# Kernel optimization log

Measured on AMD Instinct MI355X. Metric: run time of the kernel, lower is better.

The kernel has to match this reference:

```python
import jax, jax.numpy as jnp
import numpy as np

B, C, H, W = 16, 128, 128, 128
K = 3          # kernel_size
RED = 8        # CA reduction


def setup_inputs() -> dict:
    key = jax.random.key(0)
    ks = jax.random.split(key, 8)
    s = 0.05
    return {
        "x0": jax.random.normal(ks[0], (B, C, H, W), jnp.float32),
        "deg": jax.random.normal(ks[1], (B, C), jnp.float32),
        # kernel-generating MLP (torch Linear weights: (out, in), no bias)
        "w1": jax.random.normal(ks[2], (C, C), jnp.float32) * s,
        "w2": jax.random.normal(ks[3], (C * K * K, C), jnp.float32) * s,
        # 1x1 conv (with bias)
        "conv_w": jax.random.normal(ks[4], (C, C, 1, 1), jnp.float32) * s,
        "conv_b": jax.random.normal(ks[5], (C,), jnp.float32) * s,
        # CA layer 1x1 convs (no bias)
        "ca_w1": jax.random.normal(ks[6], (C // RED, C, 1, 1), jnp.float32) * s,
        "ca_w2": jax.random.normal(ks[7], (C, C // RED, 1, 1), jnp.float32) * s,
    }


def _lrelu(v):
    return jax.nn.leaky_relu(v, 0.1)


def reference(x0, deg, w1, w2, conv_w, conv_b, ca_w1, ca_w2):
    b, c, h, w = x0.shape
    # dynamic per-sample depthwise kernels: (b, C*K*K) -> (b*C, 1, K, K)
    kern = (_lrelu(deg @ w1.T) @ w2.T).reshape(b * c, 1, K, K)
    pad = (K - 1) // 2
    # grouped conv with groups = b*c (per-sample depthwise)
    out = jax.lax.conv_general_dilated(
        x0.reshape(1, b * c, h, w), kern,
        window_strides=(1, 1), padding=[(pad, pad), (pad, pad)],
        feature_group_count=b * c,
        dimension_numbers=("NCHW", "OIHW", "NCHW"))
    out = _lrelu(out).reshape(b, c, h, w)
    # 1x1 conv with bias
    out = jnp.einsum("bchw,oc->bohw", out, conv_w[:, :, 0, 0]) + conv_b[None, :, None, None]
    # CA attention from degradation rep (all 1x1 convs on a 1x1 map == matmuls)
    att = jax.nn.sigmoid(
        jnp.einsum("br,or->bo", _lrelu(jnp.einsum("bc,rc->br", deg, ca_w1[:, :, 0, 0])),
                   ca_w2[:, :, 0, 0]))
    return out + x0 * att[:, :, None, None]
```

## Files before the change

### kernel.cpp

```cpp
#include <hip/hip_runtime.h>
#include <hip/hip_bf16.h>
#include <stdint.h>

static constexpr int BB = 16, CC_ = 128, HH = 128, WW = 128;

typedef float  f32x4 __attribute__((ext_vector_type(4)));
typedef short  s16x8 __attribute__((ext_vector_type(8)));
typedef uint32_t u32x4 __attribute__((ext_vector_type(4)));

__device__ __forceinline__ uint16_t f2bf(float f) {
    union { float f; uint32_t u; } a; a.f = f;
    uint32_t r = a.u + 0x7FFFu + ((a.u >> 16) & 1u);
    return (uint16_t)(r >> 16);
}

__device__ __forceinline__ float lrelu(float v) { return fmaxf(v, 0.1f * v); }

__global__ __launch_bounds__(128) void prep_kernel(
    const float* __restrict__ deg, const float* __restrict__ w1,
    const float* __restrict__ w2, const float* __restrict__ conv_w,
    const float* __restrict__ ca_w1, const float* __restrict__ ca_w2,
    float* __restrict__ kern_ws, float* __restrict__ att_ws,
    uint16_t* __restrict__ Wp)
{
    const int t = threadIdx.x;
    if (blockIdx.x < 16) {
        const int b = blockIdx.x;
        __shared__ float sdeg[128];
        __shared__ float shid[128];
        __shared__ float sh2[16];
        sdeg[t] = deg[b * 128 + t];
        __syncthreads();
        {
            float acc = 0.f;
            const float* w1r = w1 + t * 128;
            for (int c = 0; c < 128; ++c) acc += sdeg[c] * w1r[c];
            shid[t] = lrelu(acc);
        }
        if (t < 16) {
            float a2 = 0.f;
            const float* cw = ca_w1 + t * 128;
            for (int c = 0; c < 128; ++c) a2 += sdeg[c] * cw[c];
            sh2[t] = lrelu(a2);
        }
        __syncthreads();
        {
            float aa = 0.f;
            const float* c2 = ca_w2 + t * 16;
            #pragma unroll
            for (int r = 0; r < 16; ++r) aa += sh2[r] * c2[r];
            att_ws[b * 128 + t] = 1.f / (1.f + expf(-aa));
        }
        for (int j = 0; j < 9; ++j) {
            float kv = 0.f;
            const float* w2r = w2 + (t * 9 + j) * 128;
            for (int r = 0; r < 128; ++r) kv += shid[r] * w2r[r];
            kern_ws[(b * 128 + t) * 12 + j] = kv;
        }
        kern_ws[(b * 128 + t) * 12 + 9]  = 0.f;
        kern_ws[(b * 128 + t) * 12 + 10] = 0.f;
        kern_ws[(b * 128 + t) * 12 + 11] = 0.f;
    } else {
        for (int idx = t; idx < 16384; idx += 128) {
            int j    = idx & 7;
            int lane = (idx >> 3) & 63;
            int kk   = (idx >> 9) & 3;
            int mt   = idx >> 11;
            int o = mt * 16 + (lane & 15);
            int c = kk * 32 + ((lane >> 4) & 3) * 8 + j;
            Wp[idx] = f2bf(conv_w[o * 128 + c]);
        }
    }
}

__global__ __launch_bounds__(256, 2) void main_kernel(
    const float* __restrict__ x0, const float* __restrict__ kern_ws,
    const float* __restrict__ att_ws, const uint16_t* __restrict__ Wp,
    const float* __restrict__ conv_b, float* __restrict__ out)
{
    __shared__ uint16_t y_s[128 * 128];

    const int bid = blockIdx.x;
    const int lg  = (bid & 7) * 256 + (bid >> 3);
    const int b = lg >> 7;
    const int h = lg & 127;

    const int t    = threadIdx.x;
    const int lane = t & 63;
    const int q    = t >> 6;
    const int c0   = (t >> 4) * 8;
    const int w0   = (t & 15) * 8;

    float kf[8][9];
    #pragma unroll
    for (int cc = 0; cc < 8; ++cc) {
        const float* kp = kern_ws + (b * 128 + c0 + cc) * 12;
        f32x4 ka = *(const f32x4*)kp;
        f32x4 kb = *(const f32x4*)(kp + 4);
        float k8 = kp[8];
        kf[cc][0] = ka.x; kf[cc][1] = ka.y; kf[cc][2] = ka.z; kf[cc][3] = ka.w;
        kf[cc][4] = kb.x; kf[cc][5] = kb.y; kf[cc][6] = kb.z; kf[cc][7] = kb.w;
        kf[cc][8] = k8;
    }

    uint32_t ypk[8][4];
    #pragma unroll
    for (int cc = 0; cc < 8; ++cc) {
        const int c = c0 + cc;
        const float* xpl = x0 + (b * 128 + c) * (128 * 128);
        float a8[8];
        #pragma unroll
        for (int i = 0; i < 8; ++i) a8[i] = 0.f;
        #pragma unroll
        for (int dr = 0; dr < 3; ++dr) {
            const int r = h - 1 + dr;
            f32x4 f0, f1;
            if ((unsigned)r < 128u) {
                const float* rp = xpl + r * 128 + w0;
                f0 = *(const f32x4*)rp;
                f1 = *(const f32x4*)(rp + 4);
            } else {
                f0.x = f0.y = f0.z = f0.w = 0.f;
                f1.x = f1.y = f1.z = f1.w = 0.f;
            }
            float lft = __shfl(f1.w, (lane - 1) & 63);
            float rgt = __shfl(f0.x, (lane + 1) & 63);
            if ((t & 15) == 0)  lft = 0.f;
            if ((t & 15) == 15) rgt = 0.f;
            const float k0 = kf[cc][dr * 3 + 0];
            const float k1 = kf[cc][dr * 3 + 1];
            const float k2 = kf[cc][dr * 3 + 2];
            a8[0] += k0 * lft  + k1 * f0.x + k2 * f0.y;
            a8[1] += k0 * f0.x + k1 * f0.y + k2 * f0.z;
            a8[2] += k0 * f0.y + k1 * f0.z + k2 * f0.w;
            a8[3] += k0 * f0.z + k1 * f0.w + k2 * f1.x;
            a8[4] += k0 * f0.w + k1 * f1.x + k2 * f1.y;
            a8[5] += k0 * f1.x + k1 * f1.y + k2 * f1.z;
            a8[6] += k0 * f1.y + k1 * f1.z + k2 * f1.w;
            a8[7] += k0 * f1.z + k1 * f1.w + k2 * rgt;
        }
        #pragma unroll
        for (int wi = 0; wi < 8; ++wi) {
            uint32_t u = f2bf(lrelu(a8[wi]));
            if ((cc & 1) == 0) ypk[wi][cc >> 1] = u;
            else               ypk[wi][cc >> 1] |= (u << 16);
        }
    }
    #pragma unroll
    for (int wi = 0; wi < 8; ++wi) {
        const int w = w0 + wi;
        int off = w * 256 + c0 * 2;
        off ^= (((w & 7) ^ ((w >> 3) & 7)) << 4);
        u32x4 v; v.x = ypk[wi][0]; v.y = ypk[wi][1]; v.z = ypk[wi][2]; v.w = ypk[wi][3];
        *(u32x4*)((char*)y_s + off) = v;
    }

    const int ah = q >> 1;
    const int nh = q & 1;
    s16x8 Af[4][4];
    #pragma unroll
    for (int mt = 0; mt < 4; ++mt)
        #pragma unroll
        for (int kk = 0; kk < 4; ++kk)
            Af[mt][kk] = *(const s16x8*)(Wp + (((ah * 4 + mt) * 4 + kk) * 64 + lane) * 8);

    float cbv[4][4], atv[4][4];
    #pragma unroll
    for (int mt = 0; mt < 4; ++mt)
        #pragma unroll
        for (int r = 0; r < 4; ++r) {
            const int o = (ah * 4 + mt) * 16 + (lane >> 4) * 4 + r;
            cbv[mt][r] = conv_b[o];
            atv[mt][r] = att_ws[b * 128 + o];
        }

    __syncthreads();

    f32x4 acc[4][4];
    #pragma unroll
    for (int mt = 0; mt < 4; ++mt)
        #pragma unroll
        for (int nt = 0; nt < 4; ++nt) {
            acc[mt][nt].x = cbv[mt][0];
            acc[mt][nt].y = cbv[mt][1];
            acc[mt][nt].z = cbv[mt][2];
            acc[mt][nt].w = cbv[mt][3];
        }

    #pragma unroll
    for (int nt = 0; nt < 4; ++nt) {
        const int w = (nh * 4 + nt) * 16 + (lane & 15);
        const int swz = (((w & 7) ^ ((w >> 3) & 7)) << 4);
        #pragma unroll
        for (int kk = 0; kk < 4; ++kk) {
            const int off = (w * 256 + kk * 64 + (lane >> 4) * 16) ^ swz;
            s16x8 Bf = *(const s16x8*)((const char*)y_s + off);
            #pragma unroll
            for (int mt = 0; mt < 4; ++mt)
                acc[mt][nt] = __builtin_amdgcn_mfma_f32_16x16x32_bf16(
                    Af[mt][kk], Bf, acc[mt][nt], 0, 0, 0);
        }
    }

    #pragma unroll
    for (int mt = 0; mt < 4; ++mt)
        #pragma unroll
        for (int nt = 0; nt < 4; ++nt) {
            const int w = (nh * 4 + nt) * 16 + (lane & 15);
            #pragma unroll
            for (int r = 0; r < 4; ++r) {
                const int o = (ah * 4 + mt) * 16 + (lane >> 4) * 4 + r;
                const int idx = ((b * 128 + o) * 128 + h) * 128 + w;
                out[idx] = acc[mt][nt][r] + x0[idx] * atv[mt][r];
            }
        }
}

extern "C" void kernel_launch(void* const* d_in, const int* in_sizes, int n_in,
                              void* d_out, int out_size, void* d_ws, size_t ws_size,
                              hipStream_t stream) {
    const float* x0     = (const float*)d_in[0];
    const float* deg    = (const float*)d_in[1];
    const float* w1     = (const float*)d_in[2];
    const float* w2     = (const float*)d_in[3];
    const float* conv_w = (const float*)d_in[4];
    const float* conv_b = (const float*)d_in[5];
    const float* ca_w1  = (const float*)d_in[6];
    const float* ca_w2  = (const float*)d_in[7];
    float* out = (float*)d_out;

    float* kern_ws = (float*)d_ws;
    float* att_ws  = kern_ws + 16 * 128 * 12;
    uint16_t* Wp   = (uint16_t*)(att_ws + 16 * 128);

    prep_kernel<<<17, 128, 0, stream>>>(deg, w1, w2, conv_w, ca_w1, ca_w2,
                                        kern_ws, att_ws, Wp);
    main_kernel<<<2048, 256, 0, stream>>>(x0, kern_ws, att_ws, Wp, conv_b, out);
}
```

Baseline: 432.7 us.

## Split prep kernel, stage epilogue through LDS for coalesced stores, raise occupancy

The serial per-sample w2 projection is moved out of the 17-block prep kernel into a second, wider kernel that uses vectorized row dot products. In the main kernel the MFMA operand roles are swapped so the output tile lands in LDS as [o][w]. It is then written back in two halves with 16-byte coalesced loads of x0 and stores to out, replacing scattered scalar accesses. Launch bounds rise to 4 blocks per SM, which trades more barriers and register pressure for occupancy and an extra kernel launch.

```diff
diff --git a/kernel.cpp b/kernel.cpp
--- a/kernel.cpp
+++ b/kernel.cpp
@@ -1,8 +1,6 @@
 #include <hip/hip_runtime.h>
 #include <hip/hip_bf16.h>
 #include <stdint.h>
-
-static constexpr int BB = 16, CC_ = 128, HH = 128, WW = 128;
 
 typedef float  f32x4 __attribute__((ext_vector_type(4)));
 typedef short  s16x8 __attribute__((ext_vector_type(8)));
@@ -13,21 +11,19 @@
     uint32_t r = a.u + 0x7FFFu + ((a.u >> 16) & 1u);
     return (uint16_t)(r >> 16);
 }
-
 __device__ __forceinline__ float lrelu(float v) { return fmaxf(v, 0.1f * v); }
 
-__global__ __launch_bounds__(128) void prep_kernel(
+__global__ __launch_bounds__(128) void prep1_kernel(
     const float* __restrict__ deg, const float* __restrict__ w1,
-    const float* __restrict__ w2, const float* __restrict__ conv_w,
-    const float* __restrict__ ca_w1, const float* __restrict__ ca_w2,
-    float* __restrict__ kern_ws, float* __restrict__ att_ws,
+    const float* __restrict__ conv_w, const float* __restrict__ ca_w1,
+    const float* __restrict__ ca_w2,
+    float* __restrict__ hid_ws, float* __restrict__ att_ws,
     uint16_t* __restrict__ Wp)
 {
     const int t = threadIdx.x;
     if (blockIdx.x < 16) {
         const int b = blockIdx.x;
         __shared__ float sdeg[128];
-        __shared__ float shid[128];
         __shared__ float sh2[16];
         sdeg[t] = deg[b * 128 + t];
         __syncthreads();
@@ -35,7 +31,7 @@
             float acc = 0.f;
             const float* w1r = w1 + t * 128;
             for (int c = 0; c < 128; ++c) acc += sdeg[c] * w1r[c];
-            shid[t] = lrelu(acc);
+            hid_ws[b * 128 + t] = lrelu(acc);
         }
         if (t < 16) {
             float a2 = 0.f;
@@ -51,34 +47,54 @@
             for (int r = 0; r < 16; ++r) aa += sh2[r] * c2[r];
             att_ws[b * 128 + t] = 1.f / (1.f + expf(-aa));
         }
-        for (int j = 0; j < 9; ++j) {
-            float kv = 0.f;
-            const float* w2r = w2 + (t * 9 + j) * 128;
-            for (int r = 0; r < 128; ++r) kv += shid[r] * w2r[r];
-            kern_ws[(b * 128 + t) * 12 + j] = kv;
-        }
-        kern_ws[(b * 128 + t) * 12 + 9]  = 0.f;
-        kern_ws[(b * 128 + t) * 12 + 10] = 0.f;
-        kern_ws[(b * 128 + t) * 12 + 11] = 0.f;
     } else {
         for (int idx = t; idx < 16384; idx += 128) {
             int j    = idx & 7;
             int lane = (idx >> 3) & 63;
             int kk   = (idx >> 9) & 3;
-            int mt   = idx >> 11;
-            int o = mt * 16 + (lane & 15);
+            int ot   = idx >> 11;
+            int o = ot * 16 + (lane & 15);
             int c = kk * 32 + ((lane >> 4) & 3) * 8 + j;
             Wp[idx] = f2bf(conv_w[o * 128 + c]);
         }
     }
 }
 
-__global__ __launch_bounds__(256, 2) void main_kernel(
+__global__ __launch_bounds__(256) void prep2_kernel(
+    const float* __restrict__ hid_ws, const float* __restrict__ w2,
+    float* __restrict__ kern_ws)
+{
+    const int b  = blockIdx.x;
+    const int cj = blockIdx.y * 256 + threadIdx.x;
+    __shared__ f32x4 shid[32];
+    if (threadIdx.x < 32)
+        shid[threadIdx.x] = *(const f32x4*)(hid_ws + b * 128 + threadIdx.x * 4);
+    __syncthreads();
+    if (cj < 1152) {
+        const int c = cj / 9, j = cj - c * 9;
+        const f32x4* row = (const f32x4*)(w2 + cj * 128);
+        float acc = 0.f;
+        #pragma unroll 8
+        for (int r = 0; r < 32; ++r) {
+            f32x4 a = shid[r], v = row[r];
+            acc += a.x * v.x + a.y * v.y + a.z * v.z + a.w * v.w;
+        }
+        kern_ws[(b * 128 + c) * 12 + j] = acc;
+    } else {
+        const int z = cj - 1152;
+        const int c = z / 3, j = 9 + (z - (z / 3) * 3);
+        kern_ws[(b * 128 + c) * 12 + j] = 0.f;
+    }
+}
+
+__global__ __launch_bounds__(256, 4) void main_kernel(
     const float* __restrict__ x0, const float* __restrict__ kern_ws,
     const float* __restrict__ att_ws, const uint16_t* __restrict__ Wp,
     const float* __restrict__ conv_b, float* __restrict__ out)
 {
-    __shared__ uint16_t y_s[128 * 128];
+    __shared__ char smem[64 * 132 * 4];
+    uint16_t* y_s   = (uint16_t*)smem;
+    float*    ystage = (float*)smem;
 
     const int bid = blockIdx.x;
     const int lg  = (bid & 7) * 256 + (bid >> 3);
@@ -97,10 +113,9 @@
         const float* kp = kern_ws + (b * 128 + c0 + cc) * 12;
         f32x4 ka = *(const f32x4*)kp;
         f32x4 kb = *(const f32x4*)(kp + 4);
-        float k8 = kp[8];
         kf[cc][0] = ka.x; kf[cc][1] = ka.y; kf[cc][2] = ka.z; kf[cc][3] = ka.w;
         kf[cc][4] = kb.x; kf[cc][5] = kb.y; kf[cc][6] = kb.z; kf[cc][7] = kb.w;
-        kf[cc][8] = k8;
+        kf[cc][8] = kp[8];
     }
 
     uint32_t ypk[8][4];
@@ -155,65 +170,78 @@
         *(u32x4*)((char*)y_s + off) = v;
     }
 
-    const int ah = q >> 1;
-    const int nh = q & 1;
-    s16x8 Af[4][4];
+    const int mh = q >> 1;
+    const int oh = q & 1;
+    s16x8 Bf[4][4];
+    #pragma unroll
+    for (int nt = 0; nt < 4; ++nt)
+        #pragma unroll
+        for (int kk = 0; kk < 4; ++kk)
+            Bf[nt][kk] = *(const s16x8*)(Wp + (((oh * 4 + nt) * 4 + kk) * 64 + lane) * 8);
+    float cb[4];
+    #pragma unroll
+    for (int nt = 0; nt < 4; ++nt)
+        cb[nt] = conv_b[(oh * 4 + nt) * 16 + (lane & 15)];
+
+    __syncthreads();
+
+    f32x4 acc[4][4];
     #pragma unroll
     for (int mt = 0; mt < 4; ++mt)
         #pragma unroll
-        for (int kk = 0; kk < 4; ++kk)
-            Af[mt][kk] = *(const s16x8*)(Wp + (((ah * 4 + mt) * 4 + kk) * 64 + lane) * 8);
-
-    float cbv[4][4], atv[4][4];
-    #pragma unroll
-    for (int mt = 0; mt < 4; ++mt)
-        #pragma unroll
-        for (int r = 0; r < 4; ++r) {
-            const int o = (ah * 4 + mt) * 16 + (lane >> 4) * 4 + r;
-            cbv[mt][r] = conv_b[o];
-            atv[mt][r] = att_ws[b * 128 + o];
-        }
-
-    __syncthreads();
-
-    f32x4 acc[4][4];
-    #pragma unroll
-    for (int mt = 0; mt < 4; ++mt)
-        #pragma unroll
         for (int nt = 0; nt < 4; ++nt) {
-            acc[mt][nt].x = cbv[mt][0];
-            acc[mt][nt].y = cbv[mt][1];
-            acc[mt][nt].z = cbv[mt][2];
-            acc[mt][nt].w = cbv[mt][3];
-        }
-
-    #pragma unroll
-    for (int nt = 0; nt < 4; ++nt) {
-        const int w = (nh * 4 + nt) * 16 + (lane & 15);
+            acc[mt][nt].x = cb[nt]; acc[mt][nt].y = cb[nt];
+            acc[mt][nt].z = cb[nt]; acc[mt][nt].w = cb[nt];
+        }
+
+    #pragma unroll
+    for (int mt = 0; mt < 4; ++mt) {
+        const int w = (mh * 4 + mt) * 16 + (lane & 15);
         const int swz = (((w & 7) ^ ((w >> 3) & 7)) << 4);
         #pragma unroll
         for (int kk = 0; kk < 4; ++kk) {
             const int off = (w * 256 + kk * 64 + (lane >> 4) * 16) ^ swz;
-            s16x8 Bf = *(const s16x8*)((const char*)y_s + off);
+            s16x8 Af = *(const s16x8*)((const char*)y_s + off);
+            #pragma unroll
+            for (int nt = 0; nt < 4; ++nt)
+                acc[mt][nt] = __builtin_amdgcn_mfma_f32_16x16x32_bf16(
+                    Af, Bf[nt][kk], acc[mt][nt], 0, 0, 0);
+        }
+    }
+
+    __syncthreads();
+
+    const int w0s = (lane >> 4) * 4;
+    #pragma unroll
+    for (int p = 0; p < 2; ++p) {
+        if (oh == p) {
             #pragma unroll
             for (int mt = 0; mt < 4; ++mt)
-                acc[mt][nt] = __builtin_amdgcn_mfma_f32_16x16x32_bf16(
-                    Af[mt][kk], Bf, acc[mt][nt], 0, 0, 0);
-        }
-    }
-
-    #pragma unroll
-    for (int mt = 0; mt < 4; ++mt)
-        #pragma unroll
-        for (int nt = 0; nt < 4; ++nt) {
-            const int w = (nh * 4 + nt) * 16 + (lane & 15);
-            #pragma unroll
-            for (int r = 0; r < 4; ++r) {
-                const int o = (ah * 4 + mt) * 16 + (lane >> 4) * 4 + r;
-                const int idx = ((b * 128 + o) * 128 + h) * 128 + w;
-                out[idx] = acc[mt][nt][r] + x0[idx] * atv[mt][r];
-            }
-        }
+                #pragma unroll
+                for (int nt = 0; nt < 4; ++nt) {
+                    const int o_loc = nt * 16 + (lane & 15);
+                    const int wrow  = (mh * 4 + mt) * 16 + w0s;
+                    *(f32x4*)&ystage[o_loc * 132 + wrow] = acc[mt][nt];
+                }
+        }
+        __syncthreads();
+        #pragma unroll
+        for (int i = 0; i < 8; ++i) {
+            const int chunk = t + 256 * i;
+            const int o_loc = chunk >> 5;
+            const int w4    = (chunk & 31) * 4;
+            f32x4 v = *(const f32x4*)&ystage[o_loc * 132 + w4];
+            const int o   = p * 64 + o_loc;
+            const int idx = ((b * 128 + o) * 128 + h) * 128 + w4;
+            f32x4 xr = *(const f32x4*)&x0[idx];
+            const float a = att_ws[b * 128 + o];
+            f32x4 rr;
+            rr.x = v.x + xr.x * a; rr.y = v.y + xr.y * a;
+            rr.z = v.z + xr.z * a; rr.w = v.w + xr.w * a;
+            *(f32x4*)&out[idx] = rr;
+        }
+        __syncthreads();
+    }
 }
 
 extern "C" void kernel_launch(void* const* d_in, const int* in_sizes, int n_in,
@@ -231,9 +259,11 @@
 
     float* kern_ws = (float*)d_ws;
     float* att_ws  = kern_ws + 16 * 128 * 12;
-    uint16_t* Wp   = (uint16_t*)(att_ws + 16 * 128);
-
-    prep_kernel<<<17, 128, 0, stream>>>(deg, w1, w2, conv_w, ca_w1, ca_w2,
-                                        kern_ws, att_ws, Wp);
+    float* hid_ws  = att_ws + 16 * 128;
+    uint16_t* Wp   = (uint16_t*)(hid_ws + 16 * 128);
+
+    prep1_kernel<<<17, 128, 0, stream>>>(deg, w1, conv_w, ca_w1, ca_w2,
+                                         hid_ws, att_ws, Wp);
+    prep2_kernel<<<dim3(16, 6), 256, 0, stream>>>(hid_ws, w2, kern_ws);
     main_kernel<<<2048, 256, 0, stream>>>(x0, kern_ws, att_ws, Wp, conv_b, out);
 }
```

Result: slower. 575.1 us (+32.9%).
